# Kernel optimization log

Hardware: AMD Instinct MI355X
Metric: run time of the kernel (lower is better)

The kernel has to match this reference:

```python
import jax, jax.numpy as jnp
import numpy as np

D_MODEL = 1024
N_HEADS = 16
D_HEAD = D_MODEL // N_HEADS
BSZ, SEQ = 1, 4096


def setup_inputs() -> dict:
    key = jax.random.key(0)
    ks = jax.random.split(key, 7)
    scale = 1.0 / np.sqrt(D_MODEL)
    q = jax.random.normal(ks[0], (BSZ, SEQ, D_MODEL), dtype=jnp.float32)
    k = jax.random.normal(ks[1], (BSZ, SEQ, D_MODEL), dtype=jnp.float32)
    v = jax.random.normal(ks[2], (BSZ, SEQ, D_MODEL), dtype=jnp.float32)
    Wq = jax.random.normal(ks[3], (D_MODEL, D_MODEL), dtype=jnp.float32) * scale
    Wk = jax.random.normal(ks[4], (D_MODEL, D_MODEL), dtype=jnp.float32) * scale
    Wv = jax.random.normal(ks[5], (D_MODEL, D_MODEL), dtype=jnp.float32) * scale
    Wo = jax.random.normal(ks[6], (D_MODEL, D_MODEL), dtype=jnp.float32) * scale
    # causal mask: 1 = attend, 0 = masked (matches torch masked_fill(mask == 0, -inf))
    mask = jnp.tril(jnp.ones((SEQ, SEQ), dtype=jnp.int32))[None, None, :, :]
    return {"q": q, "k": k, "v": v, "mask": mask, "Wq": Wq, "Wk": Wk, "Wv": Wv, "Wo": Wo}


def reference(q, k, v, mask, Wq, Wk, Wv, Wo):
    bsz, seq, _ = q.shape
    # nn.Linear(d,d,bias=False): y = x @ W.T
    Q = (q @ Wq.T).reshape(bsz, seq, N_HEADS, D_HEAD).transpose(0, 2, 1, 3)
    K = (k @ Wk.T).reshape(bsz, seq, N_HEADS, D_HEAD).transpose(0, 2, 1, 3)
    V = (v @ Wv.T).reshape(bsz, seq, N_HEADS, D_HEAD).transpose(0, 2, 1, 3)
    scores = jnp.einsum("bhqd,bhkd->bhqk", Q, K) / np.sqrt(D_HEAD).astype(np.float32)
    scores = jnp.where(mask == 0, -jnp.inf, scores)
    attn = jax.nn.softmax(scores, axis=-1)
    out = jnp.einsum("bhqk,bhkd->bhqd", attn, V)
    out = out.transpose(0, 2, 1, 3).reshape(bsz, seq, D_MODEL)
    return out @ Wo.T
```

## Files before the change

kernel.cpp:

```cpp
#include <hip/hip_runtime.h>


typedef __attribute__((ext_vector_type(8))) short bf16x8;
typedef __attribute__((ext_vector_type(4))) float f32x4;
typedef __attribute__((ext_vector_type(16))) float f32x16;

#define S_LEN 4096
#define DM 1024
#define NH 16
#define DH 64

static __device__ __forceinline__ unsigned short f2bf(float f) {
  union { float f; unsigned u; } x; x.f = f;
  unsigned u = x.u;
  u += 0x7fffu + ((u >> 16) & 1u);
  return (unsigned short)(u >> 16);
}

static __device__ __forceinline__ unsigned pk2(float lo, float hi) {
  unsigned r;
  asm("v_cvt_pk_bf16_f32 %0, %1, %2" : "=v"(r) : "v"(lo), "v"(hi));
  return r;
}

static __device__ __forceinline__ float exp2_(float x) {
#if __has_builtin(__builtin_amdgcn_exp2f)
  return __builtin_amdgcn_exp2f(x);
#else
  return exp2f(x);
#endif
}

#define GLL16(gsrc, ldst)                                                      \
  __builtin_amdgcn_global_load_lds(                                            \
      (const __attribute__((address_space(1))) void*)(gsrc),                   \
      (__attribute__((address_space(3))) void*)(ldst), 16, 0, 0)

struct CastArgs {
  const float* src[8];
  unsigned short* dst[8];
  int n[8];
  float scl[8];
};

__global__ __launch_bounds__(256) void cast_all(CastArgs a) {
  int which = blockIdx.y;
  const float* __restrict__ src = a.src[which];
  unsigned short* __restrict__ dst = a.dst[which];
  int n = a.n[which];
  float s = a.scl[which];
  int i = (blockIdx.x * 256 + threadIdx.x) * 8;
  if (i >= n) return;
  f32x4 v0 = *(const f32x4*)(src + i);
  f32x4 v1 = *(const f32x4*)(src + i + 4);
  union { bf16x8 v; unsigned short u[8]; } o;
#pragma unroll
  for (int j = 0; j < 4; j++) { o.u[j] = f2bf(v0[j] * s); o.u[4 + j] = f2bf(v1[j] * s); }
  *(bf16x8*)(dst + i) = o.v;
}

static __device__ __forceinline__ void gemm_body(
    const unsigned short* __restrict__ A, const unsigned short* __restrict__ B,
    void* __restrict__ Cout, int mode, unsigned short* As, unsigned short* Bs) {
  const int K = 1024;
  int tid = threadIdx.x;
  int wid = tid >> 6, lane = tid & 63;
  int m0 = blockIdx.y * 128, n0 = blockIdx.x * 128;
  int wr = (wid >> 1) * 64, wc = (wid & 1) * 64;
  int g = lane >> 4, r = lane & 15;

  const int srow = wid * 8 + (lane >> 3);
  const int scol = 8 * ((lane & 7) ^ ((lane >> 3) & 7));
  const unsigned short* gA[4];
  const unsigned short* gB[4];
#pragma unroll
  for (int rr = 0; rr < 4; rr++) {
    gA[rr] = A + (size_t)(m0 + rr * 32 + srow) * K + scol;
    gB[rr] = B + (size_t)(n0 + rr * 32 + srow) * K + scol;
  }

  f32x4 acc[4][4] = {};
  const int rsw = (r & 7) << 3;

  for (int k0 = 0; k0 < K; k0 += 64) {
#pragma unroll
    for (int rr = 0; rr < 4; rr++) {
      GLL16(gA[rr] + k0, As + wid * 512 + rr * 2048);
      GLL16(gB[rr] + k0, Bs + wid * 512 + rr * 2048);
    }
    __syncthreads();

#pragma unroll
    for (int kk = 0; kk < 64; kk += 32) {
      bf16x8 af[4], bfr[4];
#pragma unroll
      for (int mi = 0; mi < 4; mi++)
        af[mi] = *(const bf16x8*)&As[(wr + mi * 16 + r) * 64 + ((kk + g * 8) ^ rsw)];
#pragma unroll
      for (int ni = 0; ni < 4; ni++)
        bfr[ni] = *(const bf16x8*)&Bs[(wc + ni * 16 + r) * 64 + ((kk + g * 8) ^ rsw)];
#pragma unroll
      for (int mi = 0; mi < 4; mi++)
#pragma unroll
        for (int ni = 0; ni < 4; ni++)
          acc[mi][ni] = __builtin_amdgcn_mfma_f32_16x16x32_bf16(
              af[mi], bfr[ni], acc[mi][ni], 0, 0, 0);
    }
    __syncthreads();
  }

  if (mode == 0) {
    float* C = (float*)Cout;
#pragma unroll
    for (int mi = 0; mi < 4; mi++) {
      int row = m0 + wr + mi * 16 + g * 4;
#pragma unroll
      for (int ni = 0; ni < 4; ni++) {
        int c = n0 + wc + ni * 16 + r;
#pragma unroll
        for (int j = 0; j < 4; j++)
          C[(size_t)(row + j) * DM + c] = acc[mi][ni][j];
      }
    }
  } else if (mode == 1) {
    unsigned short* Cb = (unsigned short*)Cout;
#pragma unroll
    for (int mi = 0; mi < 4; mi++) {
      int row = m0 + wr + mi * 16 + g * 4;
#pragma unroll
      for (int ni = 0; ni < 4; ni++) {
        int c = n0 + wc + ni * 16 + r;
        int h = c >> 6, d = c & 63;
#pragma unroll
        for (int j = 0; j < 4; j++)
          Cb[(size_t)h * (S_LEN * DH) + (size_t)(row + j) * DH + d] =
              f2bf(acc[mi][ni][j]);
      }
    }
  } else {
    unsigned short* Cb = (unsigned short*)Cout;
#pragma unroll
    for (int mi = 0; mi < 4; mi++) {
      int row = m0 + wr + mi * 16 + g * 4;
#pragma unroll
      for (int ni = 0; ni < 4; ni++) {
        int c = n0 + wc + ni * 16 + r;
        int h = c >> 6, d = c & 63;
#pragma unroll
        for (int j = 0; j < 4; j++) {
          int s = row + j;
          Cb[(size_t)h * (S_LEN * DH) + (size_t)(s >> 6) * 4096 + d * 64 + (s & 63)] =
              f2bf(acc[mi][ni][j]);
        }
      }
    }
  }
}

struct ProjArgs {
  const unsigned short* A[3];
  const unsigned short* B[3];
  unsigned short* C[3];
  int mode[3];
};

__global__ __launch_bounds__(256, 2) void gemm_proj(ProjArgs p) {
  __shared__ unsigned short As[8192];
  __shared__ unsigned short Bs[8192];
  int z = blockIdx.z;
  gemm_body(p.A[z], p.B[z], p.C[z], p.mode[z], As, Bs);
}

__global__ __launch_bounds__(256, 2) void gemm_one(
    const unsigned short* __restrict__ A, const unsigned short* __restrict__ B,
    void* __restrict__ Cout, int mode) {
  __shared__ unsigned short As[8192];
  __shared__ unsigned short Bs[8192];
  gemm_body(A, B, Cout, mode, As, Bs);
}

__global__ __launch_bounds__(512, 4) void attn_fwd(
    const unsigned short* __restrict__ Qh, const unsigned short* __restrict__ Kh,
    const unsigned short* __restrict__ V4, unsigned short* __restrict__ O) {
  __shared__ char smem[65536];

  const int b = blockIdx.x;
  const int hd = b & 15;
  const int t = b >> 4;
  const int qe = (t < 16) ? (31 - 2 * t) : (2 * (t - 16));
  const int q0 = qe * 128;
  const int nt = qe + 1;

  const int tid = threadIdx.x;
  const int gg = tid >> 8;
  const int ww = (tid >> 6) & 3;
  const int lane = tid & 63;
  const int l31 = lane & 31, hi = lane >> 5;
  const int qi = ww;
  const int qw = q0 + qi * 32;
  const int qrow = qw + l31;
  const int sw = (l31 & 7) << 4;

  const unsigned short* Qb = Qh + (size_t)hd * (S_LEN * DH);
  const char* Kb = (const char*)(Kh + (size_t)hd * (S_LEN * DH));
  const char* Vb = (const char*)(V4 + (size_t)hd * (S_LEN * DH));

  bf16x8 qf[4];
#pragma unroll
  for (int m = 0; m < 4; m++)
    qf[m] = *(const bf16x8*)&Qb[(size_t)qrow * DH + m * 16 + hi * 8];

  const int roleV = (ww >= 2);
  const int wv = ww & 1;
  const char* gb = roleV ? Vb : Kb;
  int soff[4];
#pragma unroll
  for (int q2 = 0; q2 < 4; q2++) {
    int rowl = wv * 32 + q2 * 8 + (lane >> 3);
    int cb = ((lane & 7) * 16) ^ (((lane >> 3) & 7) << 4);
    soff[q2] = rowl * 128 + cb;
  }
  const int ldsc = gg * 32768 + roleV * 8192 + wv * 4096;

  f32x16 oacc[2] = {};
  float m_r = -1e30f, l_r = 0.f;

  {
    const char* gp = gb + (long)(gg * nt) * 8192;
#pragma unroll
    for (int q2 = 0; q2 < 4; q2++)
      GLL16(gp + soff[q2], smem + ldsc + q2 * 1024);
  }
  __syncthreads();

  int db = 0;
  for (int it = 0; it < nt; ++it) {
    if (it + 1 < nt) {
      const char* gp = gb + (long)(gg * nt + it + 1) * 8192;
      char* lb = smem + ldsc + (db ^ 1) * 16384;
#pragma unroll
      for (int q2 = 0; q2 < 4; q2++)
        GLL16(gp + soff[q2], lb + q2 * 1024);
    }
    const int kv0 = (gg * nt + it) * 64;
    const char* Kc = smem + gg * 32768 + db * 16384;
    const char* Vc = Kc + 8192;

    if (kv0 <= qw + 31) {
      const bool hiP = (kv0 + 32 <= qw + 31);
      const bool interior = (kv0 + 63 <= qw);
      f32x16 s0 = {}, s1 = {};
#pragma unroll
      for (int m = 0; m < 4; m++) {
        bf16x8 kf = *(const bf16x8*)(Kc + l31 * 128 + ((m * 32 + hi * 16) ^ sw));
        s0 = __builtin_amdgcn_mfma_f32_32x32x16_bf16(kf, qf[m], s0, 0, 0, 0);
      }
      if (hiP) {
#pragma unroll
        for (int m = 0; m < 4; m++) {
          bf16x8 kf = *(const bf16x8*)(Kc + (32 + l31) * 128 + ((m * 32 + hi * 16) ^ sw));
          s1 = __builtin_amdgcn_mfma_f32_32x32x16_bf16(kf, qf[m], s1, 0, 0, 0);
        }
      }
      if (!interior) {
#pragma unroll
        for (int rg = 0; rg < 16; rg++) {
          const int kvl = (rg & 3) + 8 * (rg >> 2) + 4 * hi;
          s0[rg] = (kv0 + kvl <= qrow) ? s0[rg] : -1e30f;
          s1[rg] = (hiP && kv0 + 32 + kvl <= qrow) ? s1[rg] : -1e30f;
        }
      }
      float t0 = fmaxf(fmaxf(s0[0], s0[1]), s0[2]);
      float t1 = fmaxf(fmaxf(s0[3], s0[4]), s0[5]);
      float t2 = fmaxf(fmaxf(s0[6], s0[7]), s0[8]);
      float t3 = fmaxf(fmaxf(s0[9], s0[10]), s0[11]);
      float t4 = fmaxf(fmaxf(s0[12], s0[13]), s0[14]);
      float t5 = fmaxf(fmaxf(s0[15], s1[0]), s1[1]);
      float t6 = fmaxf(fmaxf(s1[2], s1[3]), s1[4]);
      float t7 = fmaxf(fmaxf(s1[5], s1[6]), s1[7]);
      float t8 = fmaxf(fmaxf(s1[8], s1[9]), s1[10]);
      float t9 = fmaxf(fmaxf(s1[11], s1[12]), s1[13]);
      float ta = fmaxf(s1[14], s1[15]);
      float u0 = fmaxf(fmaxf(t0, t1), t2);
      float u1 = fmaxf(fmaxf(t3, t4), t5);
      float u2 = fmaxf(fmaxf(t6, t7), t8);
      float u3 = fmaxf(t9, ta);
      float mx = fmaxf(fmaxf(u0, u1), fmaxf(u2, u3));
      mx = fmaxf(mx, __shfl_xor(mx, 32, 64));
      if (__any(mx > m_r + 10.0f)) {
        float mnew = fmaxf(m_r, mx);
        float sc = exp2_(m_r - mnew);
        m_r = mnew;
        l_r *= sc;
#pragma unroll
        for (int dt = 0; dt < 2; dt++)
#pragma unroll
          for (int rg = 0; rg < 16; rg++) oacc[dt][rg] *= sc;
      }
#pragma unroll
      for (int rg = 0; rg < 16; rg++) {
        s0[rg] = exp2_(s0[rg] - m_r);
        s1[rg] = exp2_(s1[rg] - m_r);
      }
      float r0 = (s0[0] + s0[1]) + (s0[2] + s0[3]);
      float r1 = (s0[4] + s0[5]) + (s0[6] + s0[7]);
      float r2 = (s0[8] + s0[9]) + (s0[10] + s0[11]);
      float r3 = (s0[12] + s0[13]) + (s0[14] + s0[15]);
      float r4 = (s1[0] + s1[1]) + (s1[2] + s1[3]);
      float r5 = (s1[4] + s1[5]) + (s1[6] + s1[7]);
      float r6 = (s1[8] + s1[9]) + (s1[10] + s1[11]);
      float r7 = (s1[12] + s1[13]) + (s1[14] + s1[15]);
      float rs = ((r0 + r1) + (r2 + r3)) + ((r4 + r5) + (r6 + r7));
      rs += __shfl_xor(rs, 32, 64);
      l_r += rs;
#pragma unroll
      for (int c = 0; c < 2; c++) {
        if (c == 0 || hiP) {
          const f32x16 P = c ? s1 : s0;
          uint2 pk[4], pp[4];
#pragma unroll
          for (int blk = 0; blk < 4; blk++) {
            pk[blk].x = pk2(P[blk * 4 + 0], P[blk * 4 + 1]);
            pk[blk].y = pk2(P[blk * 4 + 2], P[blk * 4 + 3]);
            pp[blk].x = (unsigned)__shfl_xor((int)pk[blk].x, 32, 64);
            pp[blk].y = (unsigned)__shfl_xor((int)pk[blk].y, 32, 64);
          }
#pragma unroll
          for (int n = 0; n < 2; n++) {
            union { unsigned w[4]; bf16x8 v; } u;
            u.w[0] = hi ? pp[2 * n + 1].x : pk[2 * n].x;
            u.w[1] = hi ? pp[2 * n + 1].y : pk[2 * n].y;
            u.w[2] = hi ? pk[2 * n + 1].x : pp[2 * n].x;
            u.w[3] = hi ? pk[2 * n + 1].y : pp[2 * n].y;
#pragma unroll
            for (int dt = 0; dt < 2; dt++) {
              bf16x8 vf = *(const bf16x8*)(Vc + (dt * 32 + l31) * 128 +
                            ((c * 64 + n * 32 + hi * 16) ^ sw));
              oacc[dt] = __builtin_amdgcn_mfma_f32_32x32x16_bf16(
                  vf, u.v, oacc[dt], 0, 0, 0);
            }
          }
        }
      }
    }
    __syncthreads();
    db ^= 1;
  }

  float* scr = (float*)smem;
  const int sbase = (qi * 64 + lane) * 35;
  if (gg == 1) {
#pragma unroll
    for (int dt = 0; dt < 2; dt++)
#pragma unroll
      for (int rg = 0; rg < 16; rg++) scr[sbase + dt * 16 + rg] = oacc[dt][rg];
    scr[sbase + 32] = m_r;
    scr[sbase + 33] = l_r;
  }
  __syncthreads();
  if (gg == 0) {
    float mB = scr[sbase + 32], lB = scr[sbase + 33];
    float mS = fmaxf(m_r, mB);
    float sA = exp2_(m_r - mS);
    float sB = exp2_(mB - mS);
    float rl = 1.0f / (l_r * sA + lB * sB);
    float fA = sA * rl, fB = sB * rl;
#pragma unroll
    for (int dt = 0; dt < 2; dt++)
#pragma unroll
      for (int blk = 0; blk < 4; blk++) {
        float v0 = oacc[dt][blk * 4 + 0] * fA + scr[sbase + dt * 16 + blk * 4 + 0] * fB;
        float v1 = oacc[dt][blk * 4 + 1] * fA + scr[sbase + dt * 16 + blk * 4 + 1] * fB;
        float v2 = oacc[dt][blk * 4 + 2] * fA + scr[sbase + dt * 16 + blk * 4 + 2] * fB;
        float v3 = oacc[dt][blk * 4 + 3] * fA + scr[sbase + dt * 16 + blk * 4 + 3] * fB;
        uint2 st; st.x = pk2(v0, v1); st.y = pk2(v2, v3);
        int d0 = dt * 32 + blk * 8 + 4 * hi;
        *(uint2*)&O[(size_t)qrow * DM + hd * DH + d0] = st;
      }
  }
}

extern "C" void kernel_launch(void* const* d_in, const int* in_sizes, int n_in,
                              void* d_out, int out_size, void* d_ws, size_t ws_size,
                              hipStream_t stream) {
  const float* q = (const float*)d_in[0];
  const float* k = (const float*)d_in[1];
  const float* v = (const float*)d_in[2];
  const float* Wq = (const float*)d_in[4];
  const float* Wk = (const float*)d_in[5];
  const float* Wv = (const float*)d_in[6];
  const float* Wo = (const float*)d_in[7];

  unsigned short* W = (unsigned short*)d_ws;
  const int SM = S_LEN * DM;
  const int WM = DM * DM;
  unsigned short* qb  = W;
  unsigned short* kb  = qb + SM;
  unsigned short* vb  = kb + SM;
  unsigned short* Wqb = vb + SM;
  unsigned short* Wkb = Wqb + WM;
  unsigned short* Wvb = Wkb + WM;
  unsigned short* Wob = Wvb + WM;
  unsigned short* Qh  = Wob + WM;
  unsigned short* Kh  = Qh + SM;
  unsigned short* V4  = Kh + SM;
  unsigned short* Ob  = V4 + SM;

  CastArgs ca;
  ca.src[0] = q;  ca.dst[0] = qb;  ca.n[0] = SM; ca.scl[0] = 1.f;
  ca.src[1] = k;  ca.dst[1] = kb;  ca.n[1] = SM; ca.scl[1] = 1.f;
  ca.src[2] = v;  ca.dst[2] = vb;  ca.n[2] = SM; ca.scl[2] = 1.f;
  ca.src[3] = Wq; ca.dst[3] = Wqb; ca.n[3] = WM; ca.scl[3] = 0.125f * 1.44269504f;
  ca.src[4] = Wk; ca.dst[4] = Wkb; ca.n[4] = WM; ca.scl[4] = 1.f;
  ca.src[5] = Wv; ca.dst[5] = Wvb; ca.n[5] = WM; ca.scl[5] = 1.f;
  ca.src[6] = Wo; ca.dst[6] = Wob; ca.n[6] = WM; ca.scl[6] = 1.f;
  ca.src[7] = Wo; ca.dst[7] = Wob; ca.n[7] = 0;  ca.scl[7] = 1.f;
  cast_all<<<dim3(2048, 8), 256, 0, stream>>>(ca);

  ProjArgs pa;
  pa.A[0] = qb; pa.B[0] = Wqb; pa.C[0] = Qh; pa.mode[0] = 1;
  pa.A[1] = kb; pa.B[1] = Wkb; pa.C[1] = Kh; pa.mode[1] = 1;
  pa.A[2] = vb; pa.B[2] = Wvb; pa.C[2] = V4; pa.mode[2] = 2;
  gemm_proj<<<dim3(8, 32, 3), 256, 0, stream>>>(pa);

  attn_fwd<<<dim3(512), 512, 0, stream>>>(Qh, Kh, V4, Ob);

  gemm_one<<<dim3(8, 32), 256, 0, stream>>>(Ob, Wob, d_out, 0);
}
```

Before: 133.5 us.

## Use fixed-offset softmax with lazy rescale, permlane swap, and early V loads

Replaces the running-max online softmax with a fixed offset (initial m_r = 16). Exponentials are computed before any max reduction, and rescaling happens only when a probability exceeds 1024; the rescale divides by the row maximum and folds its log2 into m_r. The per-iteration cross-half row-sum shuffle is deferred to a single shuffle after the loop. The shfl_xor-based P repacking is replaced with v_permlane32_swap, and the first V fragments are loaded before the mask and softmax to hide LDS latency. This relies on score ranges staying within fp32 and bf16 range under the fixed offset, and it holds more registers for the preloaded V fragments.

```diff
diff --git a/kernel.cpp b/kernel.cpp
--- a/kernel.cpp
+++ b/kernel.cpp
@@ -21,6 +21,10 @@
   unsigned r;
   asm("v_cvt_pk_bf16_f32 %0, %1, %2" : "=v"(r) : "v"(lo), "v"(hi));
   return r;
+}
+
+static __device__ __forceinline__ void swap32u(unsigned& a, unsigned& b) {
+  asm("v_permlane32_swap_b32 %0, %1" : "+v"(a), "+v"(b));
 }
 
 static __device__ __forceinline__ float exp2_(float x) {
@@ -223,7 +227,7 @@
   const int ldsc = gg * 32768 + roleV * 8192 + wv * 4096;
 
   f32x16 oacc[2] = {};
-  float m_r = -1e30f, l_r = 0.f;
+  float m_r = 16.0f, l_r = 0.f;
 
   {
     const char* gp = gb + (long)(gg * nt) * 8192;
@@ -262,6 +266,13 @@
           s1 = __builtin_amdgcn_mfma_f32_32x32x16_bf16(kf, qf[m], s1, 0, 0, 0);
         }
       }
+      bf16x8 vf0[4];
+#pragma unroll
+      for (int i = 0; i < 4; i++) {
+        const int dt = i >> 1, n = i & 1;
+        vf0[i] = *(const bf16x8*)(Vc + (dt * 32 + l31) * 128 +
+                   ((n * 32 + hi * 16) ^ sw));
+      }
       if (!interior) {
 #pragma unroll
         for (int rg = 0; rg < 16; rg++) {
@@ -269,6 +280,11 @@
           s0[rg] = (kv0 + kvl <= qrow) ? s0[rg] : -1e30f;
           s1[rg] = (hiP && kv0 + 32 + kvl <= qrow) ? s1[rg] : -1e30f;
         }
+      }
+#pragma unroll
+      for (int rg = 0; rg < 16; rg++) {
+        s0[rg] = exp2_(s0[rg] - m_r);
+        s1[rg] = exp2_(s1[rg] - m_r);
       }
       float t0 = fmaxf(fmaxf(s0[0], s0[1]), s0[2]);
       float t1 = fmaxf(fmaxf(s0[3], s0[4]), s0[5]);
@@ -285,22 +301,18 @@
       float u1 = fmaxf(fmaxf(t3, t4), t5);
       float u2 = fmaxf(fmaxf(t6, t7), t8);
       float u3 = fmaxf(t9, ta);
-      float mx = fmaxf(fmaxf(u0, u1), fmaxf(u2, u3));
-      mx = fmaxf(mx, __shfl_xor(mx, 32, 64));
-      if (__any(mx > m_r + 10.0f)) {
-        float mnew = fmaxf(m_r, mx);
-        float sc = exp2_(m_r - mnew);
-        m_r = mnew;
+      float mxp = fmaxf(fmaxf(u0, u1), fmaxf(u2, u3));
+      if (__any(mxp > 1024.0f)) {
+        float mrow = fmaxf(mxp, __shfl_xor(mxp, 32, 64));
+        float sc = 1.0f / mrow;
+        m_r += __log2f(mrow);
         l_r *= sc;
 #pragma unroll
+        for (int rg = 0; rg < 16; rg++) { s0[rg] *= sc; s1[rg] *= sc; }
+#pragma unroll
         for (int dt = 0; dt < 2; dt++)
 #pragma unroll
           for (int rg = 0; rg < 16; rg++) oacc[dt][rg] *= sc;
-      }
-#pragma unroll
-      for (int rg = 0; rg < 16; rg++) {
-        s0[rg] = exp2_(s0[rg] - m_r);
-        s1[rg] = exp2_(s1[rg] - m_r);
       }
       float r0 = (s0[0] + s0[1]) + (s0[2] + s0[3]);
       float r1 = (s0[4] + s0[5]) + (s0[6] + s0[7]);
@@ -310,32 +322,26 @@
       float r5 = (s1[4] + s1[5]) + (s1[6] + s1[7]);
       float r6 = (s1[8] + s1[9]) + (s1[10] + s1[11]);
       float r7 = (s1[12] + s1[13]) + (s1[14] + s1[15]);
-      float rs = ((r0 + r1) + (r2 + r3)) + ((r4 + r5) + (r6 + r7));
-      rs += __shfl_xor(rs, 32, 64);
-      l_r += rs;
+      l_r += ((r0 + r1) + (r2 + r3)) + ((r4 + r5) + (r6 + r7));
 #pragma unroll
       for (int c = 0; c < 2; c++) {
         if (c == 0 || hiP) {
           const f32x16 P = c ? s1 : s0;
-          uint2 pk[4], pp[4];
-#pragma unroll
-          for (int blk = 0; blk < 4; blk++) {
-            pk[blk].x = pk2(P[blk * 4 + 0], P[blk * 4 + 1]);
-            pk[blk].y = pk2(P[blk * 4 + 2], P[blk * 4 + 3]);
-            pp[blk].x = (unsigned)__shfl_xor((int)pk[blk].x, 32, 64);
-            pp[blk].y = (unsigned)__shfl_xor((int)pk[blk].y, 32, 64);
-          }
 #pragma unroll
           for (int n = 0; n < 2; n++) {
+            unsigned a0 = pk2(P[8 * n + 0], P[8 * n + 1]);
+            unsigned a1 = pk2(P[8 * n + 2], P[8 * n + 3]);
+            unsigned b0 = pk2(P[8 * n + 4], P[8 * n + 5]);
+            unsigned b1 = pk2(P[8 * n + 6], P[8 * n + 7]);
+            swap32u(a0, b0);
+            swap32u(a1, b1);
             union { unsigned w[4]; bf16x8 v; } u;
-            u.w[0] = hi ? pp[2 * n + 1].x : pk[2 * n].x;
-            u.w[1] = hi ? pp[2 * n + 1].y : pk[2 * n].y;
-            u.w[2] = hi ? pk[2 * n + 1].x : pp[2 * n].x;
-            u.w[3] = hi ? pk[2 * n + 1].y : pp[2 * n].y;
+            u.w[0] = a0; u.w[1] = a1; u.w[2] = b0; u.w[3] = b1;
 #pragma unroll
             for (int dt = 0; dt < 2; dt++) {
-              bf16x8 vf = *(const bf16x8*)(Vc + (dt * 32 + l31) * 128 +
-                            ((c * 64 + n * 32 + hi * 16) ^ sw));
+              bf16x8 vf = (c == 0) ? vf0[dt * 2 + n]
+                        : *(const bf16x8*)(Vc + (dt * 32 + l31) * 128 +
+                             ((64 + n * 32 + hi * 16) ^ sw));
               oacc[dt] = __builtin_amdgcn_mfma_f32_32x32x16_bf16(
                   vf, u.v, oacc[dt], 0, 0, 0);
             }
@@ -346,6 +352,8 @@
     __syncthreads();
     db ^= 1;
   }
+
+  l_r += __shfl_xor(l_r, 32, 64);
 
   float* scr = (float*)smem;
   const int sbase = (qi * 64 + lane) * 35;
```

Result: faster. 125.6 us (-5.9%).
